# Kernel optimization log

Hardware: AMD Instinct MI355X
Metric: run time of the kernel (lower is better)

Reference implementation:

```python
import jax, jax.numpy as jnp
import numpy as np

N = 100000   # nodes
E = 1600000  # edges
IN = 128     # input_dim
H = 64       # hidden_dim
OUT = 2      # output_dim
G = 64       # number of graphs in the batch


def setup_inputs() -> dict:
    key = jax.random.key(0)
    ks = jax.random.split(key, 12)
    x = jax.random.normal(ks[0], (N, IN), dtype=jnp.float32)
    edge_index = jax.random.randint(ks[1], (2, E), 0, N, dtype=jnp.int64)
    batch = jnp.sort(jax.random.randint(ks[2], (N,), 0, G, dtype=jnp.int64))
    s = 0.05
    return {
        "x": x,
        "edge_index": edge_index,
        "batch": batch,
        "W1": jax.random.normal(ks[3], (IN, H), dtype=jnp.float32) * s,
        "b1": jnp.zeros((H,), dtype=jnp.float32),
        "W2": jax.random.normal(ks[4], (H, H), dtype=jnp.float32) * s,
        "b2": jnp.zeros((H,), dtype=jnp.float32),
        "W3": jax.random.normal(ks[5], (H, H), dtype=jnp.float32) * s,
        "b3": jnp.zeros((H,), dtype=jnp.float32),
        "Wm1": jax.random.normal(ks[6], (H, H), dtype=jnp.float32) * s,
        "bm1": jnp.zeros((H,), dtype=jnp.float32),
        "Wm2": jax.random.normal(ks[7], (H, OUT), dtype=jnpp.float32) * s if False else jax.random.normal(ks[7], (H, OUT), dtype=jnp.float32) * s,
        "bm2": jnp.zeros((OUT,), dtype=jnp.float32),
    }


def _gcn_conv(x, W, b, src, dst, norm, n_nodes):
    # PyG GCNConv: h = x @ W; message = norm * h[src]; scatter-add at dst; + bias
    h = x @ W                                  # [N, H]
    msg = h[src] * norm[:, None]               # [E+N, H] gather + scale
    out = jax.ops.segment_sum(msg, dst, num_segments=n_nodes)
    return out + b


def reference(x, edge_index, batch, W1, b1, W2, b2, W3, b3, Wm1, bm1, Wm2, bm2):
    n = x.shape[0]
    # add self-loops (PyG GCNConv default add_self_loops=True)
    loop = jnp.arange(n, dtype=edge_index.dtype)
    src = jnp.concatenate([edge_index[0], loop])
    dst = jnp.concatenate([edge_index[1], loop])
    # symmetric normalization deg^-1/2 (deg over target nodes, incl. self-loops)
    deg = jax.ops.segment_sum(jnp.ones_like(dst, dtype=x.dtype), dst, num_segments=n)
    dinv = jnp.where(deg > 0, jax.lax.rsqrt(deg), 0.0)
    norm = dinv[src] * dinv[dst]               # [E+N]

    h = jax.nn.relu(_gcn_conv(x, W1, b1, src, dst, norm, n))   # dropout: eval -> identity
    h = jax.nn.relu(_gcn_conv(h, W2, b2, src, dst, norm, n))
    h = jax.nn.relu(_gcn_conv(h, W3, b3, src, dst, norm, n))

    # global_mean_pool over batch ids
    sums = jax.ops.segment_sum(h, batch, num_segments=G)       # [G, H]
    cnts = jax.ops.segment_sum(jnp.ones((n,), dtype=h.dtype), batch, num_segments=G)
    pooled = sums / jnp.maximum(cnts, 1.0)[:, None]

    # MLP head: Linear -> ReLU -> (Dropout eval) -> Linear
    z = jax.nn.relu(pooled @ Wm1 + bm1)
    return z @ Wm2 + bm2                                       # [G, OUT]
```

## Files before the change

kernel.cpp:

```cpp
#include <hip/hip_runtime.h>
#include <hip/hip_bf16.h>

#define NNODES 100000
#define NEDGES 1600000
#define IND 128
#define HD 64
#define OUTD 2
#define NG 64
#define BINSHIFT 9
#define BINSZ 512
#define BSTRIDE 12288
#define PB 256

typedef __attribute__((ext_vector_type(8))) short short8v;
typedef __attribute__((ext_vector_type(4))) float floatx4;

static __device__ __forceinline__ unsigned short f2bf(float f) {
    __hip_bfloat16 h = __float2bfloat16(f);
    return *(unsigned short*)&h;
}
static __device__ __forceinline__ float bf2f(unsigned short u) {
    __hip_bfloat16 h = *(__hip_bfloat16*)&u;
    return __bfloat162float(h);
}

__global__ __launch_bounds__(1024) void binP_kernel(const int* __restrict__ src,
                                                    const int* __restrict__ dst,
                                                    int* __restrict__ binCount,
                                                    unsigned int* __restrict__ binned,
                                                    int E, int nbins,
                                                    const float* __restrict__ W1,
                                                    const float* __restrict__ W2,
                                                    const float* __restrict__ W3,
                                                    unsigned short* __restrict__ WT1,
                                                    unsigned short* __restrict__ WT2,
                                                    unsigned short* __restrict__ WT3) {
    int blk = blockIdx.x;
    int t = threadIdx.x;
    if (blk >= PB) {
        for (int i = t; i < 64 * IND + 64 * HD + 64 * HD; i += 1024) {
            if (i < 64 * IND) {
                int nn2 = i / IND, k = i - nn2 * IND;
                WT1[i] = f2bf(W1[k * 64 + nn2]);
            } else if (i < 64 * IND + 64 * HD) {
                int j = i - 64 * IND;
                int nn2 = j / HD, k = j - nn2 * HD;
                WT2[j] = f2bf(W2[k * 64 + nn2]);
            } else {
                int j = i - 64 * IND - 64 * HD;
                int nn2 = j / HD, k = j - nn2 * HD;
                WT3[j] = f2bf(W3[k * 64 + nn2]);
            }
        }
        return;
    }
    __shared__ int lh[256];
    __shared__ int lbase[256];
    if (t < 256) lh[t] = 0;
    __syncthreads();
    int ebpb = (E + PB - 1) / PB;
    int e0 = blk * ebpb;
    int e1 = min(e0 + ebpb, E);
    int dcache[8];
    int ec = 0;
    for (int e = e0 + t; e < e1; e += 1024) {
        int d = dst[e];
        dcache[ec++] = d;
        atomicAdd(&lh[d >> BINSHIFT], 1);
    }
    __syncthreads();
    if (t < nbins) {
        int c = lh[t];
        if (c > 0) lbase[t] = atomicAdd(&binCount[t], c);
        lh[t] = 0;
    }
    __syncthreads();
    ec = 0;
    for (int e = e0 + t; e < e1; e += 1024) {
        int d = dcache[ec++];
        int b = d >> BINSHIFT;
        int idx = atomicAdd(&lh[b], 1);
        binned[(size_t)b * BSTRIDE + lbase[b] + idx] =
            ((unsigned int)(d & (BINSZ - 1)) << 17) | (unsigned int)src[e];
    }
}

template <int K, bool BF16IN, bool SCALE>
static __device__ __forceinline__ void mm_body(const void* __restrict__ Xv,
                                               const unsigned short* __restrict__ WT,
                                               const float* __restrict__ dinv,
                                               unsigned short* __restrict__ Tb,
                                               int nn, int nb, int lane) {
    const int col  = lane & 15;
    const int quad = lane >> 4;
    const int m    = min(nb + col, nn - 1);

    floatx4 acc0 = {0.f, 0.f, 0.f, 0.f};
    floatx4 acc1 = {0.f, 0.f, 0.f, 0.f};
    floatx4 acc2 = {0.f, 0.f, 0.f, 0.f};
    floatx4 acc3 = {0.f, 0.f, 0.f, 0.f};

#pragma unroll
    for (int ks = 0; ks < K; ks += 32) {
        const int k0 = ks + quad * 8;
        short8v a;
        if (BF16IN) {
            a = *(const short8v*)((const unsigned short*)Xv + (size_t)m * K + k0);
        } else {
            const float* xr = (const float*)Xv + (size_t)m * K + k0;
            float4 f0 = *(const float4*)(xr);
            float4 f1 = *(const float4*)(xr + 4);
            a[0] = (short)f2bf(f0.x); a[1] = (short)f2bf(f0.y);
            a[2] = (short)f2bf(f0.z); a[3] = (short)f2bf(f0.w);
            a[4] = (short)f2bf(f1.x); a[5] = (short)f2bf(f1.y);
            a[6] = (short)f2bf(f1.z); a[7] = (short)f2bf(f1.w);
        }
        short8v b0 = *(const short8v*)(WT + (size_t)(4 * col + 0) * K + k0);
        short8v b1 = *(const short8v*)(WT + (size_t)(4 * col + 1) * K + k0);
        short8v b2 = *(const short8v*)(WT + (size_t)(4 * col + 2) * K + k0);
        short8v b3 = *(const short8v*)(WT + (size_t)(4 * col + 3) * K + k0);
        acc0 = __builtin_amdgcn_mfma_f32_16x16x32_bf16(a, b0, acc0, 0, 0, 0);
        acc1 = __builtin_amdgcn_mfma_f32_16x16x32_bf16(a, b1, acc1, 0, 0, 0);
        acc2 = __builtin_amdgcn_mfma_f32_16x16x32_bf16(a, b2, acc2, 0, 0, 0);
        acc3 = __builtin_amdgcn_mfma_f32_16x16x32_bf16(a, b3, acc3, 0, 0, 0);
    }

#pragma unroll
    for (int r = 0; r < 4; r++) {
        int node = nb + quad * 4 + r;
        if (node < nn) {
            float sc = SCALE ? dinv[node] : 1.0f;
            unsigned int lo = (unsigned int)f2bf(sc * acc0[r]) |
                              ((unsigned int)f2bf(sc * acc1[r]) << 16);
            unsigned int hi = (unsigned int)f2bf(sc * acc2[r]) |
                              ((unsigned int)f2bf(sc * acc3[r]) << 16);
            uint2 st; st.x = lo; st.y = hi;
            ((uint2*)Tb)[(size_t)node * 16 + col] = st;
        }
    }
}

__global__ __launch_bounds__(1024) void hdmm_kernel(const unsigned int* __restrict__ binned,
                                                    const int* __restrict__ binCount,
                                                    float* __restrict__ dinv,
                                                    unsigned int* __restrict__ rowinfo,
                                                    int* __restrict__ ssrc, int nbins,
                                                    const float* __restrict__ x,
                                                    const unsigned short* __restrict__ WT1,
                                                    unsigned short* __restrict__ Tb, int n) {
    __shared__ int dh[BINSZ];
    __shared__ int rp[BINSZ];
    __shared__ int wsum[4];
    __shared__ unsigned int ecl[BSTRIDE];
    int blk = blockIdx.x, t = threadIdx.x;
    int lane = t & 63, wv = t >> 6;

    if (blk >= nbins) {
        int nb = (blk - nbins) * 256 + wv * 16;
        if (nb >= n) return;
        mm_body<IND, false, false>(x, WT1, (const float*)nullptr, Tb, n, nb, lane);
        return;
    }

    int b = blk;
    if (t < BINSZ) dh[t] = 0;
    int s0 = b * BSTRIDE;
    int cnt = binCount[b];
    for (int i = t; i < cnt; i += 1024) ecl[i] = binned[s0 + i];
    __syncthreads();
    for (int i = t; i < cnt; i += 1024)
        atomicAdd(&dh[ecl[i] >> 17], 1);
    __syncthreads();
    if (t < BINSZ) {
        int node = (b << BINSHIFT) + t;
        if (node < n) dinv[node] = 1.0f / sqrtf((float)(dh[t] + 1));
    }
    int d0 = 0, d1 = 0, p = 0;
    if (t < 256) {
        d0 = (dh[2 * t] + 3) & ~3;
        d1 = (dh[2 * t + 1] + 3) & ~3;
        p = d0 + d1;
    }
    int sc = p;
#pragma unroll
    for (int d = 1; d < 64; d <<= 1) { int v = __shfl_up(sc, d, 64); if (lane >= d) sc += v; }
    if (t < 256 && lane == 63) wsum[wv] = sc;
    __syncthreads();
    if (t < 256) {
        int add = 0;
        for (int w2 = 0; w2 < wv; w2++) add += wsum[w2];
        int ex = sc - p + add;
        rp[2 * t]     = ex;
        rp[2 * t + 1] = ex + d0;
    }
    __syncthreads();
    if (t < BINSZ) {
        int node = (b << BINSHIFT) + t;
        if (node < n)
            rowinfo[node] = ((unsigned int)(s0 + rp[t]) << 10) |
                            (unsigned int)min(dh[t], 1023);
    }
    __syncthreads();
    for (int i = t; i < cnt; i += 1024) {
        unsigned int rec = ecl[i];
        int doff = rec >> 17;
        int s = rec & 0x1FFFF;
        int idx = atomicSub(&dh[doff], 1) - 1;
        ssrc[s0 + rp[doff] + idx] = s;
    }
}

template <int K>
__global__ __launch_bounds__(256) void mm_mfma_kernel(const void* __restrict__ Xv,
                                                      const unsigned short* __restrict__ WT,
                                                      const float* __restrict__ dinv,
                                                      unsigned short* __restrict__ Tb, int nn) {
    const int lane = threadIdx.x & 63;
    const int wv   = threadIdx.x >> 6;
    const int nb   = blockIdx.x * 64 + wv * 16;
    if (nb >= nn) return;
    mm_body<K, true, true>(Xv, WT, dinv, Tb, nn, nb, lane);
}

template <int SCALED>
__global__ __launch_bounds__(256) void agg_kernel(const unsigned short* __restrict__ Tb,
                                                  const unsigned int* __restrict__ rowinfo,
                                                  const int* __restrict__ ssrc,
                                                  const float* __restrict__ dinv,
                                                  const float* __restrict__ bias,
                                                  unsigned short* __restrict__ Ob, int nn) {
    int wave = __builtin_amdgcn_readfirstlane((blockIdx.x * 256 + threadIdx.x) >> 6);
    int lane = threadIdx.x & 63;
    if (wave >= nn) return;
    int n = wave;
    float dn = dinv[n];
    float self = bf2f(Tb[(size_t)n * 64 + lane]);
    float acc = SCALED ? self : dn * self;
    unsigned int info = rowinfo[n];
    int rb = (int)(info >> 10);
    int re = rb + (int)(info & 1023);
    int i = rb;
    for (; i + 16 <= re; i += 16) {
        int s[16];
#pragma unroll
        for (int k = 0; k < 16; k++) s[k] = ssrc[i + k];
        float d[16];
        if (!SCALED) {
#pragma unroll
            for (int k = 0; k < 16; k++) d[k] = dinv[s[k]];
        }
        float v[16];
#pragma unroll
        for (int k = 0; k < 16; k++) v[k] = bf2f(Tb[(size_t)s[k] * 64 + lane]);
#pragma unroll
        for (int k = 0; k < 16; k++) acc += SCALED ? v[k] : d[k] * v[k];
    }
    for (; i + 4 <= re; i += 4) {
        int s0 = ssrc[i], s1 = ssrc[i + 1], s2 = ssrc[i + 2], s3 = ssrc[i + 3];
        float d0 = 1.f, d1 = 1.f, d2 = 1.f, d3 = 1.f;
        if (!SCALED) { d0 = dinv[s0]; d1 = dinv[s1]; d2 = dinv[s2]; d3 = dinv[s3]; }
        float v0 = bf2f(Tb[(size_t)s0 * 64 + lane]);
        float v1 = bf2f(Tb[(size_t)s1 * 64 + lane]);
        float v2 = bf2f(Tb[(size_t)s2 * 64 + lane]);
        float v3 = bf2f(Tb[(size_t)s3 * 64 + lane]);
        acc += SCALED ? v0 : d0 * v0;
        acc += SCALED ? v1 : d1 * v1;
        acc += SCALED ? v2 : d2 * v2;
        acc += SCALED ? v3 : d3 * v3;
    }
    for (; i < re; i++) {
        int s = ssrc[i];
        float v = bf2f(Tb[(size_t)s * 64 + lane]);
        acc += SCALED ? v : dinv[s] * v;
    }
    float o = dn * acc + bias[lane];
    o = o > 0.f ? o : 0.f;
    Ob[(size_t)n * 64 + lane] = f2bf(o);
}

static __device__ __forceinline__ int lbound(const int* __restrict__ a, int n, int key) {
    int lo = 0, hi = n;
    while (lo < hi) { int mid = (lo + hi) >> 1; if (a[mid] < key) lo = mid + 1; else hi = mid; }
    return lo;
}

__global__ __launch_bounds__(256) void poolhead_kernel(const unsigned short* __restrict__ Hb,
                                                       const int* __restrict__ batch,
                                                       const float* __restrict__ Wm1,
                                                       const float* __restrict__ bm1,
                                                       const float* __restrict__ Wm2,
                                                       const float* __restrict__ bm2,
                                                       float* __restrict__ out, int nn) {
    __shared__ float S[4][64];
    __shared__ float P[64];
    __shared__ float Z[64];
    __shared__ int bnds[2];
    int g = blockIdx.x, tid = threadIdx.x;
    if (tid < 2) bnds[tid] = lbound(batch, nn, g + tid);
    __syncthreads();
    int n0 = bnds[0], n1 = bnds[1];
    int c = tid >> 6, j = tid & 63;
    float acc = 0.f;
    for (int n = n0 + c; n < n1; n += 4)
        acc += bf2f(Hb[(size_t)n * 64 + j]);
    S[c][j] = acc;
    __syncthreads();
    if (tid < 64) {
        float s = S[0][tid] + S[1][tid] + S[2][tid] + S[3][tid];
        float cnt = (float)(n1 - n0);
        if (cnt < 1.f) cnt = 1.f;
        P[tid] = s / cnt;
    }
    __syncthreads();
    if (tid < 64) {
        float a = bm1[tid];
#pragma unroll 8
        for (int k = 0; k < 64; ++k) a += P[k] * Wm1[k * 64 + tid];
        Z[tid] = a > 0.f ? a : 0.f;
    }
    __syncthreads();
    if (tid < OUTD) {
        float a = bm2[tid];
#pragma unroll 8
        for (int k = 0; k < 64; ++k) a += Z[k] * Wm2[k * OUTD + tid];
        out[g * OUTD + tid] = a;
    }
}

extern "C" void kernel_launch(void* const* d_in, const int* in_sizes, int n_in,
                              void* d_out, int out_size, void* d_ws, size_t ws_size,
                              hipStream_t stream) {
    const float* x    = (const float*)d_in[0];
    const int*  edge  = (const int*)d_in[1];
    const int*  batch = (const int*)d_in[2];
    const float* W1 = (const float*)d_in[3];
    const float* b1 = (const float*)d_in[4];
    const float* W2 = (const float*)d_in[5];
    const float* b2 = (const float*)d_in[6];
    const float* W3 = (const float*)d_in[7];
    const float* b3 = (const float*)d_in[8];
    const float* Wm1 = (const float*)d_in[9];
    const float* bm1 = (const float*)d_in[10];
    const float* Wm2 = (const float*)d_in[11];
    const float* bm2 = (const float*)d_in[12];

    const int N_ = in_sizes[2];
    const int E_ = in_sizes[1] / 2;
    const int* src = edge;
    const int* dst = edge + E_;
    const int nbins = (N_ + BINSZ - 1) >> BINSHIFT;

    char* w = (char*)d_ws;
    auto alloc = [&](size_t bytes) -> void* {
        void* p = (void*)w;
        w += (bytes + 255) & ~(size_t)255;
        return p;
    };
    float* dinv   = (float*)alloc((size_t)N_ * 4);
    unsigned int* rowinfo = (unsigned int*)alloc((size_t)N_ * 4);
    int*   binCount = (int*)alloc(256 * 4);
    int*   ssrc   = (int*)alloc((size_t)nbins * BSTRIDE * 4);
    unsigned int* binned = (unsigned int*)alloc((size_t)nbins * BSTRIDE * 4);
    unsigned short* Tb  = (unsigned short*)alloc((size_t)N_ * 64 * 2);
    unsigned short* hBb = (unsigned short*)alloc((size_t)N_ * 64 * 2);
    unsigned short* WT1 = (unsigned short*)alloc((size_t)64 * IND * 2);
    unsigned short* WT2 = (unsigned short*)alloc((size_t)64 * HD * 2);
    unsigned short* WT3 = (unsigned short*)alloc((size_t)64 * HD * 2);

    hipMemsetAsync(binCount, 0, 256 * 4, stream);

    binP_kernel<<<PB + 1, 1024, 0, stream>>>(src, dst, binCount, binned, E_, nbins,
                                             W1, W2, W3, WT1, WT2, WT3);

    const int mm1blk = (N_ + 255) / 256;
    hdmm_kernel<<<nbins + mm1blk, 1024, 0, stream>>>(binned, binCount, dinv, rowinfo,
                                                     ssrc, nbins, x, WT1, Tb, N_);

    const int mmblk = (N_ + 63) / 64;
    const int aggblk = (N_ + 3) / 4;

    agg_kernel<0><<<aggblk, 256, 0, stream>>>(Tb, rowinfo, ssrc, dinv, b1, hBb, N_);
    mm_mfma_kernel<HD><<<mmblk, 256, 0, stream>>>(hBb, WT2, dinv, Tb, N_);
    agg_kernel<1><<<aggblk, 256, 0, stream>>>(Tb, rowinfo, ssrc, dinv, b2, hBb, N_);
    mm_mfma_kernel<HD><<<mmblk, 256, 0, stream>>>(hBb, WT3, dinv, Tb, N_);
    agg_kernel<1><<<aggblk, 256, 0, stream>>>(Tb, rowinfo, ssrc, dinv, b3, hBb, N_);

    poolhead_kernel<<<NG, 256, 0, stream>>>(hBb, batch, Wm1, bm1, Wm2, bm2,
                                            (float*)d_out, N_);
}
```

Baseline: 432.0 us.

## Split pooling into wide atomic-reduction kernel and separate single-block MLP head

Replaces the per-graph pooling+head kernel (64 blocks) with a pool kernel that spreads contiguous node ranges across 1024 waves and accumulates per-graph sums with atomics into a zeroed buffer. A separate one-block kernel then computes counts via binary search, divides, and runs the MLP head for all graphs. The intent is to raise parallelism in the memory-bound pooling read, at the cost of an extra launch and float atomics with nondeterministic summation order.

```diff
diff --git a/kernel.cpp b/kernel.cpp
--- a/kernel.cpp
+++ b/kernel.cpp
@@ -278,52 +278,69 @@
     Ob[(size_t)n * 64 + lane] = f2bf(o);
 }
 
+__global__ __launch_bounds__(256) void pool_kernel(const unsigned short* __restrict__ Hb,
+                                                   const int* __restrict__ batch,
+                                                   float* __restrict__ pooled, int nn) {
+    int wid = (blockIdx.x * 256 + threadIdx.x) >> 6;
+    int lane = threadIdx.x & 63;
+    int nwaves = (gridDim.x * 256) >> 6;
+    int per = (nn + nwaves - 1) / nwaves;
+    int n0 = wid * per;
+    int n1 = n0 + per; if (n1 > nn) n1 = nn;
+    if (n0 >= n1) return;
+    int cur = batch[n0];
+    float acc = 0.f;
+    for (int n = n0; n < n1; ++n) {
+        int g = batch[n];
+        if (g != cur) {
+            atomicAdd(&pooled[cur * 64 + lane], acc);
+            acc = 0.f; cur = g;
+        }
+        acc += bf2f(Hb[(size_t)n * 64 + lane]);
+    }
+    atomicAdd(&pooled[cur * 64 + lane], acc);
+}
+
 static __device__ __forceinline__ int lbound(const int* __restrict__ a, int n, int key) {
     int lo = 0, hi = n;
     while (lo < hi) { int mid = (lo + hi) >> 1; if (a[mid] < key) lo = mid + 1; else hi = mid; }
     return lo;
 }
 
-__global__ __launch_bounds__(256) void poolhead_kernel(const unsigned short* __restrict__ Hb,
-                                                       const int* __restrict__ batch,
-                                                       const float* __restrict__ Wm1,
-                                                       const float* __restrict__ bm1,
-                                                       const float* __restrict__ Wm2,
-                                                       const float* __restrict__ bm2,
-                                                       float* __restrict__ out, int nn) {
-    __shared__ float S[4][64];
-    __shared__ float P[64];
-    __shared__ float Z[64];
-    __shared__ int bnds[2];
-    int g = blockIdx.x, tid = threadIdx.x;
-    if (tid < 2) bnds[tid] = lbound(batch, nn, g + tid);
-    __syncthreads();
-    int n0 = bnds[0], n1 = bnds[1];
-    int c = tid >> 6, j = tid & 63;
-    float acc = 0.f;
-    for (int n = n0 + c; n < n1; n += 4)
-        acc += bf2f(Hb[(size_t)n * 64 + j]);
-    S[c][j] = acc;
-    __syncthreads();
-    if (tid < 64) {
-        float s = S[0][tid] + S[1][tid] + S[2][tid] + S[3][tid];
-        float cnt = (float)(n1 - n0);
-        if (cnt < 1.f) cnt = 1.f;
-        P[tid] = s / cnt;
-    }
-    __syncthreads();
-    if (tid < 64) {
-        float a = bm1[tid];
+__global__ __launch_bounds__(256) void head_kernel(const float* __restrict__ pooled,
+                                                   const int* __restrict__ batch,
+                                                   const float* __restrict__ Wm1,
+                                                   const float* __restrict__ bm1,
+                                                   const float* __restrict__ Wm2,
+                                                   const float* __restrict__ bm2,
+                                                   float* __restrict__ out, int nn) {
+    __shared__ float P[NG * 64];
+    __shared__ float Z[NG * 64];
+    __shared__ int bnds[NG + 1];
+    int tid = threadIdx.x;
+    if (tid <= NG) bnds[tid] = (tid == 0) ? 0 : ((tid == NG) ? nn : lbound(batch, nn, tid));
+    __syncthreads();
+    for (int i = tid; i < NG * 64; i += 256) {
+        int g = i >> 6;
+        float c = (float)(bnds[g + 1] - bnds[g]);
+        c = c > 1.f ? c : 1.f;
+        P[i] = pooled[i] / c;
+    }
+    __syncthreads();
+    for (int i = tid; i < NG * 64; i += 256) {
+        int g = i >> 6, j = i & 63;
+        float a = bm1[j];
 #pragma unroll 8
-        for (int k = 0; k < 64; ++k) a += P[k] * Wm1[k * 64 + tid];
-        Z[tid] = a > 0.f ? a : 0.f;
-    }
-    __syncthreads();
-    if (tid < OUTD) {
-        float a = bm2[tid];
+        for (int k = 0; k < 64; ++k) a += P[g * 64 + k] * Wm1[k * 64 + j];
+        Z[i] = a > 0.f ? a : 0.f;
+    }
+    __syncthreads();
+    for (int i = tid; i < NG * OUTD; i += 256) {
+        int g = i / OUTD, o = i % OUTD;
+        float a = bm2[o];
 #pragma unroll 8
-        for (int k = 0; k < 64; ++k) a += Z[k] * Wm2[k * OUTD + tid];
-        out[g * OUTD + tid] = a;
+        for (int k = 0; k < 64; ++k) a += Z[g * 64 + k] * Wm2[k * OUTD + o];
+        out[i] = a;
     }
 }
 
@@ -356,9 +373,10 @@
         w += (bytes + 255) & ~(size_t)255;
         return p;
     };
+    int*   binCount = (int*)alloc(256 * 4);
+    float* pooled   = (float*)alloc((size_t)NG * 64 * 4);
     float* dinv   = (float*)alloc((size_t)N_ * 4);
     unsigned int* rowinfo = (unsigned int*)alloc((size_t)N_ * 4);
-    int*   binCount = (int*)alloc(256 * 4);
     int*   ssrc   = (int*)alloc((size_t)nbins * BSTRIDE * 4);
     unsigned int* binned = (unsigned int*)alloc((size_t)nbins * BSTRIDE * 4);
     unsigned short* Tb  = (unsigned short*)alloc((size_t)N_ * 64 * 2);
@@ -367,7 +385,7 @@
     unsigned short* WT2 = (unsigned short*)alloc((size_t)64 * HD * 2);
     unsigned short* WT3 = (unsigned short*)alloc((size_t)64 * HD * 2);
 
-    hipMemsetAsync(binCount, 0, 256 * 4, stream);
+    hipMemsetAsync(binCount, 0, 256 * 4 + (size_t)NG * 64 * 4, stream);
 
     binP_kernel<<<PB + 1, 1024, 0, stream>>>(src, dst, binCount, binned, E_, nbins,
                                              W1, W2, W3, WT1, WT2, WT3);
@@ -385,6 +403,7 @@
     mm_mfma_kernel<HD><<<mmblk, 256, 0, stream>>>(hBb, WT3, dinv, Tb, N_);
     agg_kernel<1><<<aggblk, 256, 0, stream>>>(Tb, rowinfo, ssrc, dinv, b3, hBb, N_);
 
-    poolhead_kernel<<<NG, 256, 0, stream>>>(hBb, batch, Wm1, bm1, Wm2, bm2,
-                                            (float*)d_out, N_);
-}
+    pool_kernel<<<256, 256, 0, stream>>>(hBb, batch, pooled, N_);
+    head_kernel<<<1, 256, 0, stream>>>(pooled, batch, Wm1, bm1, Wm2, bm2,
+                                       (float*)d_out, N_);
+}
```

Result: faster. 387.1 us (-10.4%).
